# Kernel tuning notes

Measured on AMD Instinct MI355X. Metric: run time of the kernel, lower is better.

The kernel has to match this reference:

```python
import jax, jax.numpy as jnp
import numpy as np

D_MODEL, H, D_FF = 1024, 16, 4096
D_K = D_MODEL // H
EPS = 1e-6
NEG = -1e9

def _layernorm(x, alpha, bias):
    # matches custom LayerNorm: unbiased std (torch default), scalar alpha/bias, divide by (std+eps)
    mean = jnp.mean(x, axis=-1, keepdims=True)
    std = jnp.std(x, axis=-1, keepdims=True, ddof=1)
    return alpha * ((x - mean) / (std + EPS)) + bias

def setup_inputs() -> dict:
    key = jax.random.key(0)
    ks = jax.random.split(key, 16)
    s = 0.02
    d = {
        'X': jax.random.normal(ks[0], (8, 1024, D_MODEL), dtype=jnp.float32),
        'mask': jnp.ones((8, 1, 1, 1024), dtype=jnp.int32),
        'wq': jax.random.normal(ks[1], (D_MODEL, D_MODEL), dtype=jnp.float32) * s,
        'bq': jnp.zeros((D_MODEL,), jnp.float32),
        'wk': jax.random.normal(ks[2], (D_MODEL, D_MODEL), dtype=jnp.float32) * s,
        'bk': jnp.zeros((D_MODEL,), jnp.float32),
        'wv': jax.random.normal(ks[3], (D_MODEL, D_MODEL), dtype=jnp.float32) * s,
        'bv': jnp.zeros((D_MODEL,), jnp.float32),
        'wo': jax.random.normal(ks[4], (D_MODEL, D_MODEL), dtype=jnp.float32) * s,
        'bo': jnp.zeros((D_MODEL,), jnp.float32),
        'w1': jax.random.normal(ks[5], (D_FF, D_MODEL), dtype=jnp.float32) * s,
        'b1': jnp.zeros((D_FF,), jnp.float32),
        'w2': jax.random.normal(ks[6], (D_MODEL, D_FF), dtype=jnp.float32) * s,
        'b2': jnp.zeros((D_MODEL,), jnp.float32),
        'ln1_a': jnp.ones((1,), jnp.float32), 'ln1_b': jnp.zeros((1,), jnp.float32),
        'ln2_a': jnp.ones((1,), jnp.float32), 'ln2_b': jnp.zeros((1,), jnp.float32),
    }
    return d

def reference(X, mask, wq, bq, wk, bk, wv, bv, wo, bo, w1, b1, w2, b2, ln1_a, ln1_b, ln2_a, ln2_b):
    B, S, _ = X.shape
    # --- self-attention sublayer (pre-norm residual); dropout = identity (eval) ---
    xn = _layernorm(X, ln1_a, ln1_b)
    q = (xn @ wq.T + bq).reshape(B, S, H, D_K)
    k = (xn @ wk.T + bk).reshape(B, S, H, D_K)
    v = (xn @ wv.T + bv).reshape(B, S, H, D_K)
    scores = jnp.einsum('bqhd,bkhd->bhqk', q, k) / jnp.sqrt(jnp.float32(D_K))
    scores = jnp.where(mask == 0, NEG, scores)
    attn = jax.nn.softmax(scores, axis=-1)
    ctx = jnp.einsum('bhqk,bkhd->bqhd', attn, v).reshape(B, S, D_MODEL)
    X = X + (ctx @ wo.T + bo)
    # --- feedforward sublayer (pre-norm residual) ---
    xn = _layernorm(X, ln2_a, ln2_b)
    h = jax.nn.relu(xn @ w1.T + b1)
    X = X + (h @ w2.T + b2)
    return X
```

## Files before the change

### kernel.cpp

```cpp
#include <hip/hip_runtime.h>
#include <cstdint>
#include <cstddef>

typedef float f32x4 __attribute__((ext_vector_type(4)));
typedef short bf16x8 __attribute__((ext_vector_type(8)));

typedef __attribute__((address_space(1))) void void_g;
typedef __attribute__((address_space(3))) void void_l;

__device__ __forceinline__ void gld16(const void* g, void* l) {
  __builtin_amdgcn_global_load_lds((void_g*)g, (void_l*)l, 16, 0, 0);
}

__device__ __forceinline__ unsigned short f2b(float f) {
  union { float f; uint32_t u; } c; c.f = f;
  uint32_t u = c.u;
  return (unsigned short)((u + 0x7fffu + ((u >> 16) & 1u)) >> 16);
}

__device__ __forceinline__ uint32_t cvtpk(float lo, float hi) {
  uint32_t r;
  asm("v_cvt_pk_bf16_f32 %0, %1, %2" : "=v"(r) : "v"(lo), "v"(hi));
  return r;
}

__device__ __forceinline__ float exp2_fast(float x) {
  return __builtin_exp2f(x);
}

__global__ __launch_bounds__(256) void cast_all(const float* __restrict__ w1,
                                                const float* __restrict__ w2,
                                                const float* __restrict__ wq,
                                                const float* __restrict__ wk,
                                                const float* __restrict__ wv,
                                                const float* __restrict__ wo,
                                                unsigned short* __restrict__ d1,
                                                unsigned short* __restrict__ d2,
                                                unsigned short* __restrict__ dqk,
                                                unsigned short* __restrict__ dv,
                                                unsigned short* __restrict__ dod) {
  int blk = blockIdx.x;
  const float* s;
  unsigned short* d;
  int off;
  if (blk < 4096) { s = w1; d = d1; off = blk; }
  else if (blk < 8192) { s = w2; d = d2; off = blk - 4096; }
  else if (blk < 9216) { s = wq; d = dqk; off = blk - 8192; }
  else if (blk < 10240) { s = wk; d = dqk + (1 << 20); off = blk - 9216; }
  else if (blk < 11264) { s = wv; d = dv; off = blk - 10240; }
  else { s = wo; d = dod; off = blk - 11264; }
  int i = off * 256 + threadIdx.x;
  float4 v = ((const float4*)s)[i];
  ushort4 o;
  o.x = f2b(v.x); o.y = f2b(v.y); o.z = f2b(v.z); o.w = f2b(v.w);
  ((ushort4*)d)[i] = o;
}

__global__ __launch_bounds__(256) void ln_bf16(const float* __restrict__ X,
                                               unsigned short* __restrict__ out,
                                               const float* __restrict__ alpha,
                                               const float* __restrict__ beta) {
  int row = blockIdx.x;
  int tid = threadIdx.x;
  float4 v = ((const float4*)(X + (size_t)row * 1024))[tid];
  float s = v.x + v.y + v.z + v.w;
  float q = v.x * v.x + v.y * v.y + v.z * v.z + v.w * v.w;
#pragma unroll
  for (int m = 1; m < 64; m <<= 1) { s += __shfl_xor(s, m); q += __shfl_xor(q, m); }
  __shared__ float red[8];
  int wave = tid >> 6;
  if ((tid & 63) == 0) { red[wave] = s; red[4 + wave] = q; }
  __syncthreads();
  s = red[0] + red[1] + red[2] + red[3];
  q = red[4] + red[5] + red[6] + red[7];
  float mean = s * (1.0f / 1024.0f);
  float var = fmaxf((q - 1024.0f * mean * mean) * (1.0f / 1023.0f), 0.0f);
  float inv = alpha[0] / (sqrtf(var) + 1e-6f);
  float b = beta[0];
  ushort4 o;
  o.x = f2b((v.x - mean) * inv + b);
  o.y = f2b((v.y - mean) * inv + b);
  o.z = f2b((v.z - mean) * inv + b);
  o.w = f2b((v.w - mean) * inv + b);
  ((ushort4*)(out + (size_t)row * 1024))[tid] = o;
}

template <int RELU, int BIAS2>
__global__ __launch_bounds__(512, 1) void gemm256(const unsigned short* __restrict__ A,
                                                  const unsigned short* __restrict__ W,
                                                  const float* __restrict__ bias,
                                                  const float* __restrict__ bias2, int b2off,
                                                  unsigned short* __restrict__ outB,
                                                  int M, int N, int K, int sA, int sW) {
  __shared__ unsigned short lds[2][4][128 * 64];
  int nbn = N >> 8;
  int nwg = gridDim.x;
  int bid = blockIdx.x;
  int wg = (bid & 7) * (nwg >> 3) + (bid >> 3);
  int tm = wg / nbn, tn = wg % nbn;
  int tid = threadIdx.x;
  int wave = tid >> 6, lane = tid & 63;
  int wr = wave >> 2, wc = wave & 3;
  int l15 = lane & 15, g = lane >> 4;
  int nt = K >> 6;

  const unsigned short* Abase = A + (size_t)(tm * 256) * sA;
  const unsigned short* Wbase = W + (size_t)(tn * 256) * sW;
  int srow = tid >> 3;
  int schunk = (tid & 7) ^ (srow & 7);

  f32x4 acc[8][4] = {};
  bf16x8 afrA[2][2], afrB[2][2], bfr[2][4];

  auto stage = [&](int buf, int s, int kt) {
    const unsigned short* base = (s < 2) ? Abase : Wbase;
    int str = (s < 2) ? sA : sW;
    int rbase = (s & 1) * 128;
#pragma unroll
    for (int e = 0; e < 2; ++e) {
      gld16(base + (size_t)(rbase + srow + e * 64) * str + kt * 64 + schunk * 8,
            &lds[buf][s][wave * 512 + e * 4096]);
    }
  };
  auto readB = [&](int buf) {
    const unsigned short* Bh = &lds[buf][2 + (wc >> 1)][0];
#pragma unroll
    for (int kk = 0; kk < 2; ++kk)
#pragma unroll
      for (int j = 0; j < 4; ++j) {
        int br = (wc & 1) * 64 + j * 16 + l15;
        bfr[kk][j] = *(const bf16x8*)&Bh[br * 64 + (((kk * 4 + g) ^ (br & 7)) * 8)];
      }
  };
  auto readA = [&](bf16x8 (&dst)[2][2], int buf, int q) {
    const unsigned short* Ah = &lds[buf][wr][0];
#pragma unroll
    for (int kk = 0; kk < 2; ++kk)
#pragma unroll
      for (int ri = 0; ri < 2; ++ri) {
        int ar = q * 32 + ri * 16 + l15;
        dst[kk][ri] = *(const bf16x8*)&Ah[ar * 64 + (((kk * 4 + g) ^ (ar & 7)) * 8)];
      }
  };
  auto mfma16 = [&](bf16x8 (&af)[2][2], int q) {
    __builtin_amdgcn_s_setprio(1);
#pragma unroll
    for (int kk = 0; kk < 2; ++kk)
#pragma unroll
      for (int ri = 0; ri < 2; ++ri)
#pragma unroll
        for (int j = 0; j < 4; ++j)
          acc[q * 2 + ri][j] = __builtin_amdgcn_mfma_f32_16x16x32_bf16(
              af[kk][ri], bfr[kk][j], acc[q * 2 + ri][j], 0, 0, 0);
    __builtin_amdgcn_s_setprio(0);
  };

  stage(0, 2, 0); stage(0, 3, 0); stage(0, 0, 0); stage(0, 1, 0);
  stage(1, 2, 1); stage(1, 3, 1);
  asm volatile("s_waitcnt vmcnt(4)" ::: "memory");
  __builtin_amdgcn_s_barrier();

  for (int t = 0; t < nt; ++t) {
    int buf = t & 1;
    __builtin_amdgcn_sched_barrier(0);
    if (t + 1 < nt) stage(buf ^ 1, 0, t + 1);
    readB(buf);
    readA(afrA, buf, 0);
    readA(afrB, buf, 1);
    mfma16(afrA, 0);
    __builtin_amdgcn_s_barrier();
    __builtin_amdgcn_sched_barrier(0);
    if (t + 1 < nt) stage(buf ^ 1, 1, t + 1);
    readA(afrA, buf, 2);
    mfma16(afrB, 1);
    __builtin_amdgcn_s_barrier();
    __builtin_amdgcn_sched_barrier(0);
    if (t + 2 < nt) stage(buf, 2, t + 2);
    readA(afrB, buf, 3);
    mfma16(afrA, 2);
    __builtin_amdgcn_s_barrier();
    __builtin_amdgcn_sched_barrier(0);
    if (t + 2 < nt) stage(buf, 3, t + 2);
    mfma16(afrB, 3);
    if (t + 2 < nt) asm volatile("s_waitcnt vmcnt(4)" ::: "memory");
    else asm volatile("s_waitcnt vmcnt(0)" ::: "memory");
    __builtin_amdgcn_s_barrier();
  }

  int row0 = tm * 256 + wr * 128 + g * 4;
  int col0 = tn * 256 + wc * 64 + l15;
#pragma unroll
  for (int i = 0; i < 8; ++i) {
#pragma unroll
    for (int j = 0; j < 4; ++j) {
      int col = col0 + j * 16;
      float bb = (BIAS2 && col >= b2off) ? bias2[col - b2off] : bias[col];
#pragma unroll
      for (int r = 0; r < 4; ++r) {
        int row = row0 + i * 16 + r;
        float v = acc[i][j][r] + bb;
        if (RELU) v = fmaxf(v, 0.0f);
        outB[(size_t)row * N + col] = f2b(v);
      }
    }
  }
}

template <int MODE>
__global__ __launch_bounds__(512, 1) void gemm256x128(const unsigned short* __restrict__ A,
                                                      const unsigned short* __restrict__ W,
                                                      const float* __restrict__ bias,
                                                      const float* __restrict__ resid,
                                                      float* __restrict__ outF,
                                                      unsigned short* __restrict__ outB,
                                                      int M, int N, int K, int sA, int sW) {
  __shared__ unsigned short lds[2][3][128 * 64];
  int nbn = N >> 7;
  int nwg = gridDim.x;
  int bid = blockIdx.x;
  int wg = (bid & 7) * (nwg >> 3) + (bid >> 3);
  int tm = wg / nbn, tn = wg % nbn;
  int tid = threadIdx.x;
  int wave = tid >> 6, lane = tid & 63;
  int wr = wave >> 2, wc = wave & 3;
  int l15 = lane & 15, g = lane >> 4;
  int nt = K >> 6;

  const unsigned short* Abase = A + (size_t)(tm * 256) * sA;
  const unsigned short* Wbase = W + (size_t)(tn * 128) * sW;
  int srow = tid >> 3;
  int schunk = (tid & 7) ^ (srow & 7);

  f32x4 acc[8][2] = {};
  bf16x8 afrA[2][2], afrB[2][2], bfr[2][2];

  auto stage = [&](int buf, int s, int kt) {
    const unsigned short* base = (s < 2) ? Abase : Wbase;
    int str = (s < 2) ? sA : sW;
    int rbase = (s & 1) * 128;
#pragma unroll
    for (int e = 0; e < 2; ++e) {
      gld16(base + (size_t)(rbase + srow + e * 64) * str + kt * 64 + schunk * 8,
            &lds[buf][s][wave * 512 + e * 4096]);
    }
  };
  auto readB = [&](int buf) {
    const unsigned short* Bh = &lds[buf][2][0];
#pragma unroll
    for (int kk = 0; kk < 2; ++kk)
#pragma unroll
      for (int j = 0; j < 2; ++j) {
        int br = wc * 32 + j * 16 + l15;
        bfr[kk][j] = *(const bf16x8*)&Bh[br * 64 + (((kk * 4 + g) ^ (br & 7)) * 8)];
      }
  };
  auto readA = [&](bf16x8 (&dst)[2][2], int buf, int q) {
    const unsigned short* Ah = &lds[buf][wr][0];
#pragma unroll
    for (int kk = 0; kk < 2; ++kk)
#pragma unroll
      for (int ri = 0; ri < 2; ++ri) {
        int ar = q * 32 + ri * 16 + l15;
        dst[kk][ri] = *(const bf16x8*)&Ah[ar * 64 + (((kk * 4 + g) ^ (ar & 7)) * 8)];
      }
  };
  auto mfma8 = [&](bf16x8 (&af)[2][2], int q) {
    __builtin_amdgcn_s_setprio(1);
#pragma unroll
    for (int kk = 0; kk < 2; ++kk)
#pragma unroll
      for (int ri = 0; ri < 2; ++ri)
#pragma unroll
        for (int j = 0; j < 2; ++j)
          acc[q * 2 + ri][j] = __builtin_amdgcn_mfma_f32_16x16x32_bf16(
              af[kk][ri], bfr[kk][j], acc[q * 2 + ri][j], 0, 0, 0);
    __builtin_amdgcn_s_setprio(0);
  };

  stage(0, 2, 0); stage(0, 0, 0); stage(0, 1, 0);
  stage(1, 2, 1);
  asm volatile("s_waitcnt vmcnt(2)" ::: "memory");
  __builtin_amdgcn_s_barrier();

  for (int t = 0; t < nt; ++t) {
    int buf = t & 1;
    __builtin_amdgcn_sched_barrier(0);
    if (t + 1 < nt) stage(buf ^ 1, 0, t + 1);
    readB(buf);
    readA(afrA, buf, 0);
    readA(afrB, buf, 1);
    mfma8(afrA, 0);
    __builtin_amdgcn_s_barrier();
    __builtin_amdgcn_sched_barrier(0);
    if (t + 1 < nt) stage(buf ^ 1, 1, t + 1);
    readA(afrA, buf, 2);
    mfma8(afrB, 1);
    __builtin_amdgcn_s_barrier();
    __builtin_amdgcn_sched_barrier(0);
    if (t + 2 < nt) stage(buf, 2, t + 2);
    readA(afrB, buf, 3);
    mfma8(afrA, 2);
    __builtin_amdgcn_s_barrier();
    __builtin_amdgcn_sched_barrier(0);
    mfma8(afrB, 3);
    if (t + 2 < nt) asm volatile("s_waitcnt vmcnt(2)" ::: "memory");
    else asm volatile("s_waitcnt vmcnt(0)" ::: "memory");
    __builtin_amdgcn_s_barrier();
  }

  int row0 = tm * 256 + wr * 128 + g * 4;
  int col0 = tn * 128 + wc * 32 + l15;
#pragma unroll
  for (int i = 0; i < 8; ++i) {
#pragma unroll
    for (int j = 0; j < 2; ++j) {
      int col = col0 + j * 16;
      float cb = (MODE == 2) ? bias[col] : 0.0f;
#pragma unroll
      for (int r = 0; r < 4; ++r) {
        int row = row0 + i * 16 + r;
        size_t idx = (size_t)row * N + col;
        float v = acc[i][j][r];
        if (MODE == 1) outB[idx] = f2b(v + bias[row]);
        else if (MODE == 2) outF[idx] = resid[idx] + v + cb;
        else outF[idx] += v;
      }
    }
  }
}

__global__ __launch_bounds__(512, 6) void attn_fwd7(const unsigned short* __restrict__ QK,
                                                    const unsigned short* __restrict__ Vt,
                                                    const int* __restrict__ mask,
                                                    unsigned short* __restrict__ O) {
  __shared__ unsigned short Kl[2][64 * 64];
  __shared__ unsigned short Vl[2][64 * 64];
  __shared__ float biasl[1024];
  int bid = blockIdx.x;
  int wg = (bid & 7) * 128 + (bid >> 3);
  int qt = wg & 7, bh = wg >> 3;
  int b = bh >> 4, h = bh & 15;
  int tid = threadIdx.x, wave = tid >> 6, lane = tid & 63;
  int l15 = lane & 15, g = lane >> 4;
  int q0 = qt * 128;

  for (int i = tid; i < 1024; i += 512)
    biasl[i] = (mask[b * 1024 + i] == 0) ? -1.4426950e9f : 0.0f;

  const unsigned short* Qrow = QK + ((size_t)(b * 1024 + q0 + wave * 16 + l15)) * 2048 + h * 64;
  bf16x8 qf0 = *(const bf16x8*)(Qrow + g * 8);
  bf16x8 qf1 = *(const bf16x8*)(Qrow + 32 + g * 8);

  float l_q = 0.0f;
  f32x4 o[4] = {};

  int srow = tid >> 3;
  int clog = (tid & 7) ^ (srow & 7);
  int h7 = l15 & 7;
  const float SC = 0.125f * 1.44269504f;

  auto stageKV = [&](int buf, int kt) {
    gld16(QK + ((size_t)(b * 1024 + kt * 64 + srow)) * 2048 + 1024 + h * 64 + clog * 8,
          &Kl[buf][(wave * 8) * 64]);
    gld16(Vt + ((size_t)(h * 64 + srow)) * 8192 + b * 1024 + kt * 64 + clog * 8,
          &Vl[buf][(wave * 8) * 64]);
  };

  stageKV(0, 0);
  __syncthreads();
  int cur = 0;

  for (int kt = 0; kt < 16; ++kt) {
    if (kt < 15) stageKV(cur ^ 1, kt + 1);

    f32x4 st[4];
    __builtin_amdgcn_s_setprio(1);
#pragma unroll
    for (int j = 0; j < 4; ++j) {
      int kr = j * 16 + l15;
      bf16x8 ka = *(const bf16x8*)&Kl[cur][kr * 64 + ((g ^ h7) * 8)];
      bf16x8 kb = *(const bf16x8*)&Kl[cur][kr * 64 + (((4 + g) ^ h7) * 8)];
      f32x4 z = {};
      st[j] = __builtin_amdgcn_mfma_f32_16x16x32_bf16(ka, qf0, z, 0, 0, 0);
      st[j] = __builtin_amdgcn_mfma_f32_16x16x32_bf16(kb, qf1, st[j], 0, 0, 0);
    }
    __builtin_amdgcn_s_setprio(0);

    union U8 { uint32_t u[4]; bf16x8 v; } pa[2];
#pragma unroll
    for (int j = 0; j < 4; ++j) {
      float4 b4 = *(const float4*)&biasl[kt * 64 + j * 16 + g * 4];
      float e0 = exp2_fast(st[j][0] * SC + b4.x);
      float e1 = exp2_fast(st[j][1] * SC + b4.y);
      float e2 = exp2_fast(st[j][2] * SC + b4.z);
      float e3 = exp2_fast(st[j][3] * SC + b4.w);
      l_q += (e0 + e1) + (e2 + e3);
      pa[j >> 1].u[(j & 1) * 2 + 0] = cvtpk(e0, e1);
      pa[j >> 1].u[(j & 1) * 2 + 1] = cvtpk(e2, e3);
    }

    __builtin_amdgcn_s_setprio(1);
#pragma unroll
    for (int kk = 0; kk < 2; ++kk) {
#pragma unroll
      for (int dt = 0; dt < 4; ++dt) {
        int vr = dt * 16 + l15;
        uint2 lo = *(const uint2*)&Vl[cur][vr * 64 + (((4 * kk + (g >> 1)) ^ h7) * 8) + (g & 1) * 4];
        uint2 hi = *(const uint2*)&Vl[cur][vr * 64 + (((4 * kk + 2 + (g >> 1)) ^ h7) * 8) + (g & 1) * 4];
        union U8 vbu;
        vbu.u[0] = lo.x; vbu.u[1] = lo.y; vbu.u[2] = hi.x; vbu.u[3] = hi.y;
        o[dt] = __builtin_amdgcn_mfma_f32_16x16x32_bf16(vbu.v, pa[kk].v, o[dt], 0, 0, 0);
      }
    }
    __builtin_amdgcn_s_setprio(0);

    __syncthreads();
    cur ^= 1;
  }

  l_q += __shfl_xor(l_q, 16);
  l_q += __shfl_xor(l_q, 32);
  float inv = 1.0f / l_q;
  size_t orow = ((size_t)(b * 1024 + q0 + wave * 16 + l15)) * 1024 + h * 64;
#pragma unroll
  for (int dt = 0; dt < 4; ++dt) {
    uint2 w;
    w.x = cvtpk(o[dt][0] * inv, o[dt][1] * inv);
    w.y = cvtpk(o[dt][2] * inv, o[dt][3] * inv);
    *(uint2*)&O[orow + dt * 16 + g * 4] = w;
  }
}

extern "C" void kernel_launch(void* const* d_in, const int* in_sizes, int n_in,
                              void* d_out, int out_size, void* d_ws, size_t ws_size,
                              hipStream_t stream) {
  const float* X = (const float*)d_in[0];
  const int* mask = (const int*)d_in[1];
  const float* wq = (const float*)d_in[2];
  const float* bq = (const float*)d_in[3];
  const float* wk = (const float*)d_in[4];
  const float* bk = (const float*)d_in[5];
  const float* wv = (const float*)d_in[6];
  const float* bv = (const float*)d_in[7];
  const float* wo = (const float*)d_in[8];
  const float* bo = (const float*)d_in[9];
  const float* w1 = (const float*)d_in[10];
  const float* b1 = (const float*)d_in[11];
  const float* w2 = (const float*)d_in[12];
  const float* b2 = (const float*)d_in[13];
  const float* ln1a = (const float*)d_in[14];
  const float* ln1b = (const float*)d_in[15];
  const float* ln2a = (const float*)d_in[16];
  const float* ln2b = (const float*)d_in[17];
  float* out = (float*)d_out;
  char* ws = (char*)d_ws;
  const size_t MB = 1024 * 1024;

  unsigned short* w1_b = (unsigned short*)(ws + 0 * MB);
  unsigned short* w2_b = (unsigned short*)(ws + 8 * MB);
  unsigned short* wqk_b = (unsigned short*)(ws + 16 * MB);
  unsigned short* wv_b = (unsigned short*)(ws + 20 * MB);
  unsigned short* wo_b = (unsigned short*)(ws + 22 * MB);
  unsigned short* xn = (unsigned short*)(ws + 24 * MB);
  unsigned short* QKb = (unsigned short*)(ws + 40 * MB);
  unsigned short* Vtb = (unsigned short*)(ws + 72 * MB);
  unsigned short* hb = QKb;

  cast_all<<<12288, 256, 0, stream>>>(w1, w2, wq, wk, wv, wo, w1_b, w2_b, wqk_b, wv_b, wo_b);

  ln_bf16<<<8192, 256, 0, stream>>>(X, xn, ln1a, ln1b);
  gemm256<0, 1><<<256, 512, 0, stream>>>(xn, wqk_b, bq, bk, 1024, QKb,
                                         8192, 2048, 1024, 1024, 1024);
  gemm256x128<1><<<256, 512, 0, stream>>>(wv_b, xn, bv, nullptr, nullptr, Vtb,
                                          1024, 8192, 1024, 1024, 1024);
  attn_fwd7<<<1024, 512, 0, stream>>>(QKb, Vtb, mask, xn);
  gemm256x128<2><<<256, 512, 0, stream>>>(xn, wo_b, bo, X, out, nullptr,
                                          8192, 1024, 1024, 1024, 1024);
  ln_bf16<<<8192, 256, 0, stream>>>(out, xn, ln2a, ln2b);
  for (int hc = 0; hc < 2; ++hc) {
    gemm256<1, 0><<<256, 512, 0, stream>>>(xn, w1_b + (size_t)hc * 2048 * 1024,
                                           b1 + hc * 2048, nullptr, 0, hb,
                                           8192, 2048, 1024, 1024, 1024);
    if (hc == 0)
      gemm256x128<2><<<256, 512, 0, stream>>>(hb, w2_b, b2, out, out, nullptr,
                                              8192, 1024, 2048, 2048, 4096);
    else
      gemm256x128<3><<<256, 512, 0, stream>>>(hb, w2_b + 2048, nullptr, nullptr, out, nullptr,
                                              8192, 1024, 2048, 2048, 4096);
  }
}
```

Before: 358.8 us.

## Process four query tiles per attention block to reuse staged K/V

The attention kernel now gives each block 512 query rows (four 16-row sets per wave) instead of 128, so each K/V tile loaded into LDS and each V fragment read from LDS serves four times as many queries. The grid shrinks from 1024 to 256 blocks and the launch bound drops to 2 blocks per SM to allow the extra accumulator and Q registers. This cuts global K/V traffic and LDS staging per query, at the cost of higher register pressure, lower occupancy, and fewer blocks to spread across the compute units.

```diff
diff --git a/kernel.cpp b/kernel.cpp
--- a/kernel.cpp
+++ b/kernel.cpp
@@ -329,30 +329,36 @@
   }
 }
 
-__global__ __launch_bounds__(512, 6) void attn_fwd7(const unsigned short* __restrict__ QK,
-                                                    const unsigned short* __restrict__ Vt,
-                                                    const int* __restrict__ mask,
-                                                    unsigned short* __restrict__ O) {
+__global__ __launch_bounds__(512, 2) void attn_fwd10(const unsigned short* __restrict__ QK,
+                                                     const unsigned short* __restrict__ Vt,
+                                                     const int* __restrict__ mask,
+                                                     unsigned short* __restrict__ O) {
   __shared__ unsigned short Kl[2][64 * 64];
   __shared__ unsigned short Vl[2][64 * 64];
   __shared__ float biasl[1024];
   int bid = blockIdx.x;
-  int wg = (bid & 7) * 128 + (bid >> 3);
-  int qt = wg & 7, bh = wg >> 3;
+  int wg = (bid & 7) * 32 + (bid >> 3);
+  int qt = wg & 1, bh = wg >> 1;
   int b = bh >> 4, h = bh & 15;
   int tid = threadIdx.x, wave = tid >> 6, lane = tid & 63;
   int l15 = lane & 15, g = lane >> 4;
-  int q0 = qt * 128;
+  int q0 = qt * 512;
 
   for (int i = tid; i < 1024; i += 512)
     biasl[i] = (mask[b * 1024 + i] == 0) ? -1.4426950e9f : 0.0f;
 
-  const unsigned short* Qrow = QK + ((size_t)(b * 1024 + q0 + wave * 16 + l15)) * 2048 + h * 64;
-  bf16x8 qf0 = *(const bf16x8*)(Qrow + g * 8);
-  bf16x8 qf1 = *(const bf16x8*)(Qrow + 32 + g * 8);
-
-  float l_q = 0.0f;
-  f32x4 o[4] = {};
+  const unsigned short* Qr0 = QK + ((size_t)(b * 1024 + q0 + wave * 16 + l15)) * 2048 + h * 64;
+  bf16x8 qa0 = *(const bf16x8*)(Qr0 + g * 8);
+  bf16x8 qa1 = *(const bf16x8*)(Qr0 + 32 + g * 8);
+  bf16x8 qb0 = *(const bf16x8*)(Qr0 + (size_t)128 * 2048 + g * 8);
+  bf16x8 qb1 = *(const bf16x8*)(Qr0 + (size_t)128 * 2048 + 32 + g * 8);
+  bf16x8 qc0 = *(const bf16x8*)(Qr0 + (size_t)256 * 2048 + g * 8);
+  bf16x8 qc1 = *(const bf16x8*)(Qr0 + (size_t)256 * 2048 + 32 + g * 8);
+  bf16x8 qd0 = *(const bf16x8*)(Qr0 + (size_t)384 * 2048 + g * 8);
+  bf16x8 qd1 = *(const bf16x8*)(Qr0 + (size_t)384 * 2048 + 32 + g * 8);
+
+  float l_a = 0.0f, l_b = 0.0f, l_c = 0.0f, l_d = 0.0f;
+  f32x4 oa[4] = {}, ob[4] = {}, oc[4] = {}, od[4] = {};
 
   int srow = tid >> 3;
   int clog = (tid & 7) ^ (srow & 7);
@@ -370,34 +376,46 @@
   __syncthreads();
   int cur = 0;
 
+  union U8 { uint32_t u[4]; bf16x8 v; };
+
   for (int kt = 0; kt < 16; ++kt) {
     if (kt < 15) stageKV(cur ^ 1, kt + 1);
 
-    f32x4 st[4];
-    __builtin_amdgcn_s_setprio(1);
+    bf16x8 ka[4], kb[4];
 #pragma unroll
     for (int j = 0; j < 4; ++j) {
       int kr = j * 16 + l15;
-      bf16x8 ka = *(const bf16x8*)&Kl[cur][kr * 64 + ((g ^ h7) * 8)];
-      bf16x8 kb = *(const bf16x8*)&Kl[cur][kr * 64 + (((4 + g) ^ h7) * 8)];
-      f32x4 z = {};
-      st[j] = __builtin_amdgcn_mfma_f32_16x16x32_bf16(ka, qf0, z, 0, 0, 0);
-      st[j] = __builtin_amdgcn_mfma_f32_16x16x32_bf16(kb, qf1, st[j], 0, 0, 0);
-    }
-    __builtin_amdgcn_s_setprio(0);
-
-    union U8 { uint32_t u[4]; bf16x8 v; } pa[2];
-#pragma unroll
-    for (int j = 0; j < 4; ++j) {
-      float4 b4 = *(const float4*)&biasl[kt * 64 + j * 16 + g * 4];
-      float e0 = exp2_fast(st[j][0] * SC + b4.x);
-      float e1 = exp2_fast(st[j][1] * SC + b4.y);
-      float e2 = exp2_fast(st[j][2] * SC + b4.z);
-      float e3 = exp2_fast(st[j][3] * SC + b4.w);
-      l_q += (e0 + e1) + (e2 + e3);
-      pa[j >> 1].u[(j & 1) * 2 + 0] = cvtpk(e0, e1);
-      pa[j >> 1].u[(j & 1) * 2 + 1] = cvtpk(e2, e3);
-    }
+      ka[j] = *(const bf16x8*)&Kl[cur][kr * 64 + ((g ^ h7) * 8)];
+      kb[j] = *(const bf16x8*)&Kl[cur][kr * 64 + (((4 + g) ^ h7) * 8)];
+    }
+
+    U8 pa[2], pb[2], pc[2], pd[2];
+#define QKSET(q0v, q1v, lsum, pdst)                                              \
+    {                                                                            \
+      f32x4 s_[4];                                                               \
+      __builtin_amdgcn_s_setprio(1);                                             \
+      _Pragma("unroll") for (int j = 0; j < 4; ++j) {                            \
+        f32x4 z = {};                                                            \
+        s_[j] = __builtin_amdgcn_mfma_f32_16x16x32_bf16(ka[j], q0v, z, 0, 0, 0); \
+        s_[j] = __builtin_amdgcn_mfma_f32_16x16x32_bf16(kb[j], q1v, s_[j], 0, 0, 0); \
+      }                                                                          \
+      __builtin_amdgcn_s_setprio(0);                                             \
+      _Pragma("unroll") for (int j = 0; j < 4; ++j) {                            \
+        float4 b4 = *(const float4*)&biasl[kt * 64 + j * 16 + g * 4];            \
+        float e0 = exp2_fast(s_[j][0] * SC + b4.x);                              \
+        float e1 = exp2_fast(s_[j][1] * SC + b4.y);                              \
+        float e2 = exp2_fast(s_[j][2] * SC + b4.z);                              \
+        float e3 = exp2_fast(s_[j][3] * SC + b4.w);                              \
+        lsum += (e0 + e1) + (e2 + e3);                                           \
+        pdst[j >> 1].u[(j & 1) * 2 + 0] = cvtpk(e0, e1);                         \
+        pdst[j >> 1].u[(j & 1) * 2 + 1] = cvtpk(e2, e3);                         \
+      }                                                                          \
+    }
+    QKSET(qa0, qa1, l_a, pa)
+    QKSET(qb0, qb1, l_b, pb)
+    QKSET(qc0, qc1, l_c, pc)
+    QKSET(qd0, qd1, l_d, pd)
+#undef QKSET
 
     __builtin_amdgcn_s_setprio(1);
 #pragma unroll
@@ -407,9 +425,12 @@
         int vr = dt * 16 + l15;
         uint2 lo = *(const uint2*)&Vl[cur][vr * 64 + (((4 * kk + (g >> 1)) ^ h7) * 8) + (g & 1) * 4];
         uint2 hi = *(const uint2*)&Vl[cur][vr * 64 + (((4 * kk + 2 + (g >> 1)) ^ h7) * 8) + (g & 1) * 4];
-        union U8 vbu;
+        U8 vbu;
         vbu.u[0] = lo.x; vbu.u[1] = lo.y; vbu.u[2] = hi.x; vbu.u[3] = hi.y;
-        o[dt] = __builtin_amdgcn_mfma_f32_16x16x32_bf16(vbu.v, pa[kk].v, o[dt], 0, 0, 0);
+        oa[dt] = __builtin_amdgcn_mfma_f32_16x16x32_bf16(vbu.v, pa[kk].v, oa[dt], 0, 0, 0);
+        ob[dt] = __builtin_amdgcn_mfma_f32_16x16x32_bf16(vbu.v, pb[kk].v, ob[dt], 0, 0, 0);
+        oc[dt] = __builtin_amdgcn_mfma_f32_16x16x32_bf16(vbu.v, pc[kk].v, oc[dt], 0, 0, 0);
+        od[dt] = __builtin_amdgcn_mfma_f32_16x16x32_bf16(vbu.v, pd[kk].v, od[dt], 0, 0, 0);
       }
     }
     __builtin_amdgcn_s_setprio(0);
@@ -418,17 +439,24 @@
     cur ^= 1;
   }
 
-  l_q += __shfl_xor(l_q, 16);
-  l_q += __shfl_xor(l_q, 32);
-  float inv = 1.0f / l_q;
   size_t orow = ((size_t)(b * 1024 + q0 + wave * 16 + l15)) * 1024 + h * 64;
-#pragma unroll
-  for (int dt = 0; dt < 4; ++dt) {
-    uint2 w;
-    w.x = cvtpk(o[dt][0] * inv, o[dt][1] * inv);
-    w.y = cvtpk(o[dt][2] * inv, o[dt][3] * inv);
-    *(uint2*)&O[orow + dt * 16 + g * 4] = w;
-  }
+#define EPI(lsum, ov, roff)                                                      \
+  {                                                                              \
+    lsum += __shfl_xor(lsum, 16);                                                \
+    lsum += __shfl_xor(lsum, 32);                                                \
+    float inv = 1.0f / lsum;                                                     \
+    _Pragma("unroll") for (int dt = 0; dt < 4; ++dt) {                           \
+      uint2 w;                                                                   \
+      w.x = cvtpk(ov[dt][0] * inv, ov[dt][1] * inv);                             \
+      w.y = cvtpk(ov[dt][2] * inv, ov[dt][3] * inv);                             \
+      *(uint2*)&O[orow + (size_t)(roff) * 1024 + dt * 16 + g * 4] = w;           \
+    }                                                                            \
+  }
+  EPI(l_a, oa, 0)
+  EPI(l_b, ob, 128)
+  EPI(l_c, oc, 256)
+  EPI(l_d, od, 384)
+#undef EPI
 }
 
 extern "C" void kernel_launch(void* const* d_in, const int* in_sizes, int n_in,
@@ -473,7 +501,7 @@
                                          8192, 2048, 1024, 1024, 1024);
   gemm256x128<1><<<256, 512, 0, stream>>>(wv_b, xn, bv, nullptr, nullptr, Vtb,
                                           1024, 8192, 1024, 1024, 1024);
-  attn_fwd7<<<1024, 512, 0, stream>>>(QKb, Vtb, mask, xn);
+  attn_fwd10<<<256, 512, 0, stream>>>(QKb, Vtb, mask, xn);
   gemm256x128<2><<<256, 512, 0, stream>>>(xn, wo_b, bo, X, out, nullptr,
                                           8192, 1024, 1024, 1024, 1024);
   ln_bf16<<<8192, 256, 0, stream>>>(out, xn, ln2a, ln2b);
```

Result: no change. 360.6 us (+0.5%).
